# Kernel optimization log

Measured on AMD Instinct MI355X. Metric: run time of the kernel, lower is better.

Reference implementation:

```python
import jax, jax.numpy as jnp
from jax import lax
import numpy as np

B, T, ID, HD = 64, 256, 512, 1024

def setup_inputs() -> dict:
    key = jax.random.key(0)
    ks = jax.random.split(key, 5)
    s_i = 1.0 / np.sqrt(ID)
    s_h = 1.0 / np.sqrt(HD)
    return {
        'x': jax.random.normal(ks[0], (B, T, ID), jnp.float32),
        'Wi': jax.random.uniform(ks[1], (ID, 4 * HD), jnp.float32, -s_i, s_i),
        'bi': jax.random.uniform(ks[2], (4 * HD,), jnp.float32, -s_i, s_i),
        'Wh': jax.random.uniform(ks[3], (HD, 4 * HD), jnp.float32, -s_h, s_h),
        'bh': jax.random.uniform(ks[4], (4 * HD,), jnp.float32, -s_h, s_h),
    }

def reference(x, Wi, bi, Wh, bh):
    # x: [B, T, ID]; Wi: [ID, 4H]; Wh: [HD, 4H]
    b, t, _ = x.shape
    hd = Wh.shape[0]
    # Precompute input-to-hidden contribution for all timesteps: [T, B, 4H]
    gates_x = jnp.swapaxes(jnp.einsum('bti,ih->bth', x, Wi) + bi, 0, 1)

    def step(carry, gx):
        h, c = carry
        g = gx + h @ Wh + bh  # [B, 4H]
        f, i, a, o = jnp.split(g, 4, axis=-1)  # chunk order: F, I, A, O
        f = jax.nn.sigmoid(f)
        i = jax.nn.sigmoid(i)
        a = jnp.tanh(a)
        o = jax.nn.sigmoid(o)
        c = f * c + i * a
        h = o * jnp.tanh(c)
        return (h, c), h

    h0 = jnp.zeros((b, hd), x.dtype)
    c0 = jnp.zeros((b, hd), x.dtype)
    (hT, cT), hs = lax.scan(step, (h0, c0), gates_x)
    Q_all = jnp.swapaxes(hs, 0, 1)  # [B, T, HD]
    return (Q_all, hT, cT)
```

## Files before the change

kernel.cpp:

```cpp
#include <hip/hip_runtime.h>
#include <hip/hip_bf16.h>


#define B_  64
#define T_  256
#define ID_ 512
#define HD_ 1024
#define NG_ 4096
#define M1_ (B_ * T_)
#define NBLK 64
#define UPB  16

typedef __bf16 bf16x8 __attribute__((ext_vector_type(8)));
typedef float  f32x4  __attribute__((ext_vector_type(4)));
typedef int    i32x4  __attribute__((ext_vector_type(4)));
typedef short  s16x4  __attribute__((ext_vector_type(4)));

using bf16 = __hip_bfloat16;

__device__ __forceinline__ float sigmoid_fast(float x) {
    return 1.0f / (1.0f + __expf(-x));
}
__device__ __forceinline__ float tanh_fast(float x) {
    return 1.0f - 2.0f / (__expf(2.0f * x) + 1.0f);
}
__device__ __forceinline__ unsigned short bf16_bits(float x) {
    union { bf16 h; unsigned short u; } cv;
    cv.h = __float2bfloat16(x);
    return cv.u;
}
__device__ __forceinline__ bf16x8 as_bf16x8(i32x4 v) {
    union { i32x4 i; bf16x8 h; } cv;
    cv.i = v;
    return cv.h;
}

__device__ __forceinline__ void issue8(i32x4* dst, const bf16* gbase) {
    asm volatile(
        "global_load_dwordx4 %0, %8, off sc0 sc1\n\t"
        "global_load_dwordx4 %1, %8, off offset:64 sc0 sc1\n\t"
        "global_load_dwordx4 %2, %8, off offset:128 sc0 sc1\n\t"
        "global_load_dwordx4 %3, %8, off offset:192 sc0 sc1\n\t"
        "global_load_dwordx4 %4, %8, off offset:256 sc0 sc1\n\t"
        "global_load_dwordx4 %5, %8, off offset:320 sc0 sc1\n\t"
        "global_load_dwordx4 %6, %8, off offset:384 sc0 sc1\n\t"
        "global_load_dwordx4 %7, %8, off offset:448 sc0 sc1"
        : "=&v"(dst[0]), "=&v"(dst[1]), "=&v"(dst[2]), "=&v"(dst[3]),
          "=&v"(dst[4]), "=&v"(dst[5]), "=&v"(dst[6]), "=&v"(dst[7])
        : "v"(gbase));
}

__global__ __launch_bounds__(256) void prep_kernel(
    const float* __restrict__ x, const float* __restrict__ Wi,
    const float* __restrict__ Wh, bf16* __restrict__ xb,
    bf16* __restrict__ wiT, bf16* __restrict__ whT,
    bf16* __restrict__ hbuf, int* __restrict__ flags) {
    const int tid = blockIdx.x * 256 + threadIdx.x;

    if (tid < NBLK * 4 * 16) flags[tid] = 0;
    if (tid < (B_ * HD_) / 4)
        *reinterpret_cast<s16x4*>(hbuf + (size_t)tid * 4) = s16x4{0, 0, 0, 0};

    const float4 v = reinterpret_cast<const float4*>(x)[tid];
    bf16 tmp[4] = { __float2bfloat16(v.x), __float2bfloat16(v.y),
                    __float2bfloat16(v.z), __float2bfloat16(v.w) };
    *reinterpret_cast<s16x4*>(xb + 4 * (size_t)tid) =
        *reinterpret_cast<s16x4*>(tmp);

    {
        const int n = tid >> 9, k = tid & 511;
        wiT[tid] = __float2bfloat16(Wi[(size_t)k * NG_ + n]);
    }
    for (int e = 0; e < 2; ++e) {
        const int idx = 2 * tid + e;
        const int n = idx >> 10, k = idx & 1023;
        whT[idx] = __float2bfloat16(Wh[(size_t)k * NG_ + n]);
    }
}

__global__ __launch_bounds__(256) void gates_gemm_kernel(
    const bf16* __restrict__ xb, const bf16* __restrict__ wiT,
    const float* __restrict__ bi, const float* __restrict__ bh,
    bf16* __restrict__ gates3) {
    __shared__ __align__(16) bf16 As[128 * 40];
    __shared__ __align__(16) bf16 Bs[128 * 40];
    const int tid  = threadIdx.x;
    const int lane = tid & 63, wave = tid >> 6;
    const int wm = wave >> 1, wn = wave & 1;
    const int l15 = lane & 15, quad = lane >> 4;
    const int row0 = blockIdx.x * 128, col0 = blockIdx.y * 128;

    f32x4 acc[4][4];
    for (int i = 0; i < 4; ++i)
        for (int j = 0; j < 4; ++j) acc[i][j] = f32x4{0.f, 0.f, 0.f, 0.f};

    for (int kt = 0; kt < ID_ / 32; ++kt) {
        const int k0 = kt * 32;
        for (int L = tid; L < 512; L += 256) {
            const int r = L >> 2, s = L & 3;
            *reinterpret_cast<i32x4*>(&As[r * 40 + s * 8]) =
                *reinterpret_cast<const i32x4*>(xb + (size_t)(row0 + r) * ID_ + k0 + s * 8);
            *reinterpret_cast<i32x4*>(&Bs[r * 40 + s * 8]) =
                *reinterpret_cast<const i32x4*>(wiT + (size_t)(col0 + r) * ID_ + k0 + s * 8);
        }
        __syncthreads();
        bf16x8 af[4], bfv[4];
        for (int mt = 0; mt < 4; ++mt)
            af[mt] = *reinterpret_cast<const bf16x8*>(
                &As[(wm * 64 + mt * 16 + l15) * 40 + quad * 8]);
        for (int nt = 0; nt < 4; ++nt)
            bfv[nt] = *reinterpret_cast<const bf16x8*>(
                &Bs[(wn * 64 + nt * 16 + l15) * 40 + quad * 8]);
        for (int mt = 0; mt < 4; ++mt)
            for (int nt = 0; nt < 4; ++nt)
                acc[mt][nt] = __builtin_amdgcn_mfma_f32_16x16x32_bf16(
                    af[mt], bfv[nt], acc[mt][nt], 0, 0, 0);
        __syncthreads();
    }
    for (int mt = 0; mt < 4; ++mt) {
        for (int nt = 0; nt < 4; ++nt) {
            const int cg = col0 + wn * 64 + nt * 16 + l15;
            const int g = cg >> 10, u = cg & 1023;
            const int blk = u >> 4, ul = u & 15;
            const int q2 = ul >> 2, r2 = ul & 3;
            const int e = g * 4 + r2;
            const float bias = bi[cg] + bh[cg];
            for (int r = 0; r < 4; ++r) {
                const int rg = row0 + wm * 64 + mt * 16 + quad * 4 + r;
                const int b = rg >> 8, t = rg & 255;
                const int tid2 = (b >> 4) * 64 + q2 * 16 + (b & 15);
                gates3[(((size_t)t * NBLK + blk) * 256 + tid2) * 16 + e] =
                    __float2bfloat16(acc[mt][nt][r] + bias);
            }
        }
    }
}

__global__ __launch_bounds__(256, 1) void lstm_persistent_kernel(
    const bf16* __restrict__ gates3, const bf16* __restrict__ whT,
    bf16* __restrict__ hbuf, float* __restrict__ out, int* __restrict__ flags) {
    __shared__ __align__(16) bf16 whs[32 * 4 * 64 * 8];
    const int tid  = threadIdx.x;
    const int lane = tid & 63, w = tid >> 6;
    const int l15 = lane & 15, quad = lane >> 4;
    const int blk = blockIdx.x;

    for (int c = tid; c < 8192; c += 256) {
        const int kk = c >> 8, sel = (c >> 6) & 3, ln = c & 63;
        const size_t wrow = (size_t)(sel * HD_ + blk * UPB + (ln & 15));
        const int col = (ln >> 4) * 8 + kk * 32;
        *reinterpret_cast<i32x4*>(whs + (size_t)c * 8) =
            *reinterpret_cast<const i32x4*>(whT + wrow * HD_ + col);
    }
    __syncthreads();

    const bf16* wb = whs + (size_t)lane * 8;

    const int b = w * 16 + l15;
    float cs[4] = {0.f, 0.f, 0.f, 0.f};

    const volatile int* pf = (const volatile int*)(flags + lane);

    size_t gb0 = ((size_t)blk * 256 + tid) * 16;
    bf16x8 gxa_n = *reinterpret_cast<const bf16x8*>(gates3 + gb0);
    bf16x8 gxb_n = *reinterpret_cast<const bf16x8*>(gates3 + gb0 + 8);

    for (int t = 0; t < T_; ++t) {
        const bf16* hin  = hbuf + (size_t)(t & 1) * (B_ * HD_);
        bf16*       hout = hbuf + (size_t)((t + 1) & 1) * (B_ * HD_);
        const bf16x8 gxa = gxa_n, gxb = gxb_n;

        if (t > 0) {
            if (w == 0) {
                while (*pf < t) __builtin_amdgcn_s_sleep(2);
            }
            asm volatile("s_barrier" ::: "memory");
        }

        f32x4 aFe{0.f,0.f,0.f,0.f}, aFo{0.f,0.f,0.f,0.f};
        f32x4 aIe{0.f,0.f,0.f,0.f}, aIo{0.f,0.f,0.f,0.f};
        f32x4 aAe{0.f,0.f,0.f,0.f}, aAo{0.f,0.f,0.f,0.f};
        f32x4 aOe{0.f,0.f,0.f,0.f}, aOo{0.f,0.f,0.f,0.f};

        const bf16* hb_base = hin + (size_t)b * HD_ + quad * 8;
        i32x4 hbA[8], hbB[8];

        auto consume8 = [&](const i32x4* hbg, const int kkb) {
#pragma unroll
            for (int i = 0; i < 8; i += 2) {
                const int kk = kkb + i;
                const bf16* f0 = wb + (size_t)kk * 2048;
                const bf16* f1 = f0 + 2048;
                const bf16x8 he = as_bf16x8(hbg[i]);
                const bf16x8 ho = as_bf16x8(hbg[i + 1]);
                aFe = __builtin_amdgcn_mfma_f32_16x16x32_bf16(
                    *reinterpret_cast<const bf16x8*>(f0),        he, aFe, 0, 0, 0);
                aIe = __builtin_amdgcn_mfma_f32_16x16x32_bf16(
                    *reinterpret_cast<const bf16x8*>(f0 + 512),  he, aIe, 0, 0, 0);
                aAe = __builtin_amdgcn_mfma_f32_16x16x32_bf16(
                    *reinterpret_cast<const bf16x8*>(f0 + 1024), he, aAe, 0, 0, 0);
                aOe = __builtin_amdgcn_mfma_f32_16x16x32_bf16(
                    *reinterpret_cast<const bf16x8*>(f0 + 1536), he, aOe, 0, 0, 0);
                aFo = __builtin_amdgcn_mfma_f32_16x16x32_bf16(
                    *reinterpret_cast<const bf16x8*>(f1),        ho, aFo, 0, 0, 0);
                aIo = __builtin_amdgcn_mfma_f32_16x16x32_bf16(
                    *reinterpret_cast<const bf16x8*>(f1 + 512),  ho, aIo, 0, 0, 0);
                aAo = __builtin_amdgcn_mfma_f32_16x16x32_bf16(
                    *reinterpret_cast<const bf16x8*>(f1 + 1024), ho, aAo, 0, 0, 0);
                aOo = __builtin_amdgcn_mfma_f32_16x16x32_bf16(
                    *reinterpret_cast<const bf16x8*>(f1 + 1536), ho, aOo, 0, 0, 0);
            }
        };

        issue8(hbA, hb_base);
        issue8(hbB, hb_base + 8 * 32);
        asm volatile("s_waitcnt vmcnt(8)" ::: "memory");
        __builtin_amdgcn_sched_barrier(0);
        consume8(hbA, 0);
        issue8(hbA, hb_base + 16 * 32);
        asm volatile("s_waitcnt vmcnt(8)" ::: "memory");
        __builtin_amdgcn_sched_barrier(0);
        consume8(hbB, 8);
        issue8(hbB, hb_base + 24 * 32);
        asm volatile("s_waitcnt vmcnt(8)" ::: "memory");
        __builtin_amdgcn_sched_barrier(0);
        consume8(hbA, 16);
        asm volatile("s_waitcnt vmcnt(0)" ::: "memory");
        __builtin_amdgcn_sched_barrier(0);
        consume8(hbB, 24);

        const f32x4 accF = aFe + aFo;
        const f32x4 accI = aIe + aIo;
        const f32x4 accA = aAe + aAo;
        const f32x4 accO = aOe + aOo;
        float hs[4];
#pragma unroll
        for (int r = 0; r < 4; ++r) {
            const float fv = sigmoid_fast(accF[r] + (float)gxa[r]);
            const float iv = sigmoid_fast(accI[r] + (float)gxa[4 + r]);
            const float av = tanh_fast   (accA[r] + (float)gxb[r]);
            const float ov = sigmoid_fast(accO[r] + (float)gxb[4 + r]);
            cs[r] = fv * cs[r] + iv * av;
            hs[r] = ov * tanh_fast(cs[r]);
        }

        const int hidx = b * HD_ + blk * UPB + quad * 4;
        *reinterpret_cast<float4*>(
            out + ((size_t)b * T_ + t) * HD_ + blk * UPB + quad * 4) =
            make_float4(hs[0], hs[1], hs[2], hs[3]);
        if (t == T_ - 1) {
            *reinterpret_cast<float4*>(out + (size_t)M1_ * HD_ + hidx) =
                make_float4(hs[0], hs[1], hs[2], hs[3]);
            *reinterpret_cast<float4*>(
                out + (size_t)M1_ * HD_ + B_ * HD_ + hidx) =
                make_float4(cs[0], cs[1], cs[2], cs[3]);
        }
        if (t < T_ - 1) {
            const unsigned long long hp =
                (unsigned long long)bf16_bits(hs[0]) |
                ((unsigned long long)bf16_bits(hs[1]) << 16) |
                ((unsigned long long)bf16_bits(hs[2]) << 32) |
                ((unsigned long long)bf16_bits(hs[3]) << 48);
            *reinterpret_cast<volatile unsigned long long*>(hout + hidx) = hp;
            __asm__ __volatile__("s_waitcnt vmcnt(0)" ::: "memory");
            asm volatile("s_barrier" ::: "memory");
            if (tid == 0)
                *reinterpret_cast<volatile int*>(flags + blk) = t + 1;
            __asm__ __volatile__("" ::: "memory");
            const size_t gb = (((size_t)(t + 1) * NBLK + blk) * 256 + tid) * 16;
            gxa_n = *reinterpret_cast<const bf16x8*>(gates3 + gb);
            gxb_n = *reinterpret_cast<const bf16x8*>(gates3 + gb + 8);
        }
    }
}

extern "C" void kernel_launch(void* const* d_in, const int* in_sizes, int n_in,
                              void* d_out, int out_size, void* d_ws, size_t ws_size,
                              hipStream_t stream) {
    const float* x  = (const float*)d_in[0];
    const float* Wi = (const float*)d_in[1];
    const float* bi = (const float*)d_in[2];
    const float* Wh = (const float*)d_in[3];
    const float* bh = (const float*)d_in[4];
    float* out = (float*)d_out;

    char* ws = (char*)d_ws;
    size_t off = 0;
    bf16* xb     = (bf16*)(ws + off); off += (size_t)M1_ * ID_ * 2;
    bf16* wiT    = (bf16*)(ws + off); off += (size_t)NG_ * ID_ * 2;
    bf16* whT    = (bf16*)(ws + off); off += (size_t)NG_ * HD_ * 2;
    bf16* gates3 = (bf16*)(ws + off); off += (size_t)T_ * B_ * NG_ * 2;
    bf16* hbuf   = (bf16*)(ws + off); off += (size_t)2 * B_ * HD_ * 2;
    int* flags   = (int*)(ws + off);  off += (size_t)NBLK * 4 * 16 * 4;

    prep_kernel<<<8192, 256, 0, stream>>>(x, Wi, Wh, xb, wiT, whT, hbuf, flags);
    gates_gemm_kernel<<<dim3(128, 32), 256, 0, stream>>>(xb, wiT, bi, bh, gates3);

    lstm_persistent_kernel<<<dim3(NBLK), dim3(256), 0, stream>>>(
        gates3, whT, hbuf, out, flags);
}
```

Measured before the change: 2.050 ms.

## Halve persistent LSTM block to two waves, each handling two batch tiles

The recurrent kernel now runs 128 threads per block, and each wave processes two 16-row batch tiles. Each Wh fragment read from LDS is reused across both tiles, halving LDS weight traffic per MFMA. The precomputed-gate layout is rearranged to match, giving 32 elements per thread. The spin-wait also drops its s_sleep for lower wake-up latency on the flag. In exchange each wave does twice as much serial MFMA and activation work per step, needs more registers, and the block has fewer waves to hide latency.

```diff
diff --git a/kernel.cpp b/kernel.cpp
--- a/kernel.cpp
+++ b/kernel.cpp
@@ -123,20 +123,21 @@
             const int g = cg >> 10, u = cg & 1023;
             const int blk = u >> 4, ul = u & 15;
             const int q2 = ul >> 2, r2 = ul & 3;
-            const int e = g * 4 + r2;
             const float bias = bi[cg] + bh[cg];
             for (int r = 0; r < 4; ++r) {
                 const int rg = row0 + wm * 64 + mt * 16 + quad * 4 + r;
                 const int b = rg >> 8, t = rg & 255;
-                const int tid2 = (b >> 4) * 64 + q2 * 16 + (b & 15);
-                gates3[(((size_t)t * NBLK + blk) * 256 + tid2) * 16 + e] =
+                const int w2 = b >> 5, nt2 = (b >> 4) & 1;
+                const int tid2 = w2 * 64 + q2 * 16 + (b & 15);
+                const int e = nt2 * 16 + g * 4 + r2;
+                gates3[(((size_t)t * NBLK + blk) * 128 + tid2) * 32 + e] =
                     __float2bfloat16(acc[mt][nt][r] + bias);
             }
         }
     }
 }
 
-__global__ __launch_bounds__(256, 1) void lstm_persistent_kernel(
+__global__ __launch_bounds__(128, 1) void lstm_persistent_kernel(
     const bf16* __restrict__ gates3, const bf16* __restrict__ whT,
     bf16* __restrict__ hbuf, float* __restrict__ out, int* __restrict__ flags) {
     __shared__ __align__(16) bf16 whs[32 * 4 * 64 * 8];
@@ -145,7 +146,7 @@
     const int l15 = lane & 15, quad = lane >> 4;
     const int blk = blockIdx.x;
 
-    for (int c = tid; c < 8192; c += 256) {
+    for (int c = tid; c < 8192; c += 128) {
         const int kk = c >> 8, sel = (c >> 6) & 3, ln = c & 63;
         const size_t wrow = (size_t)(sel * HD_ + blk * UPB + (ln & 15));
         const int col = (ln >> 4) * 8 + kk * 32;
@@ -156,120 +157,140 @@
 
     const bf16* wb = whs + (size_t)lane * 8;
 
-    const int b = w * 16 + l15;
-    float cs[4] = {0.f, 0.f, 0.f, 0.f};
+    const int b0 = w * 32 + l15;
+    const int b1 = b0 + 16;
+    float cs0[4] = {0.f, 0.f, 0.f, 0.f};
+    float cs1[4] = {0.f, 0.f, 0.f, 0.f};
 
     const volatile int* pf = (const volatile int*)(flags + lane);
 
-    size_t gb0 = ((size_t)blk * 256 + tid) * 16;
-    bf16x8 gxa_n = *reinterpret_cast<const bf16x8*>(gates3 + gb0);
-    bf16x8 gxb_n = *reinterpret_cast<const bf16x8*>(gates3 + gb0 + 8);
+    const bf16* gx0 = gates3 + ((size_t)blk * 128 + tid) * 32;
+    bf16x8 g0n = *reinterpret_cast<const bf16x8*>(gx0);
+    bf16x8 g1n = *reinterpret_cast<const bf16x8*>(gx0 + 8);
+    bf16x8 g2n = *reinterpret_cast<const bf16x8*>(gx0 + 16);
+    bf16x8 g3n = *reinterpret_cast<const bf16x8*>(gx0 + 24);
 
     for (int t = 0; t < T_; ++t) {
         const bf16* hin  = hbuf + (size_t)(t & 1) * (B_ * HD_);
         bf16*       hout = hbuf + (size_t)((t + 1) & 1) * (B_ * HD_);
-        const bf16x8 gxa = gxa_n, gxb = gxb_n;
+        const bf16x8 g0 = g0n, g1 = g1n, g2 = g2n, g3 = g3n;
 
         if (t > 0) {
             if (w == 0) {
-                while (*pf < t) __builtin_amdgcn_s_sleep(2);
+                while (*pf < t) {}
             }
             asm volatile("s_barrier" ::: "memory");
         }
 
-        f32x4 aFe{0.f,0.f,0.f,0.f}, aFo{0.f,0.f,0.f,0.f};
-        f32x4 aIe{0.f,0.f,0.f,0.f}, aIo{0.f,0.f,0.f,0.f};
-        f32x4 aAe{0.f,0.f,0.f,0.f}, aAo{0.f,0.f,0.f,0.f};
-        f32x4 aOe{0.f,0.f,0.f,0.f}, aOo{0.f,0.f,0.f,0.f};
-
-        const bf16* hb_base = hin + (size_t)b * HD_ + quad * 8;
-        i32x4 hbA[8], hbB[8];
-
-        auto consume8 = [&](const i32x4* hbg, const int kkb) {
+        f32x4 aF0{0.f,0.f,0.f,0.f}, aI0{0.f,0.f,0.f,0.f};
+        f32x4 aA0{0.f,0.f,0.f,0.f}, aO0{0.f,0.f,0.f,0.f};
+        f32x4 aF1{0.f,0.f,0.f,0.f}, aI1{0.f,0.f,0.f,0.f};
+        f32x4 aA1{0.f,0.f,0.f,0.f}, aO1{0.f,0.f,0.f,0.f};
+
+        const bf16* base0 = hin + (size_t)b0 * HD_ + quad * 8;
+        const bf16* base1 = hin + (size_t)b1 * HD_ + quad * 8;
+        i32x4 hbA0[8], hbA1[8], hbB0[8], hbB1[8];
+
+        auto consumePair = [&](const i32x4* h0, const i32x4* h1, const int kkb) {
 #pragma unroll
-            for (int i = 0; i < 8; i += 2) {
+            for (int i = 0; i < 8; ++i) {
                 const int kk = kkb + i;
-                const bf16* f0 = wb + (size_t)kk * 2048;
-                const bf16* f1 = f0 + 2048;
-                const bf16x8 he = as_bf16x8(hbg[i]);
-                const bf16x8 ho = as_bf16x8(hbg[i + 1]);
-                aFe = __builtin_amdgcn_mfma_f32_16x16x32_bf16(
-                    *reinterpret_cast<const bf16x8*>(f0),        he, aFe, 0, 0, 0);
-                aIe = __builtin_amdgcn_mfma_f32_16x16x32_bf16(
-                    *reinterpret_cast<const bf16x8*>(f0 + 512),  he, aIe, 0, 0, 0);
-                aAe = __builtin_amdgcn_mfma_f32_16x16x32_bf16(
-                    *reinterpret_cast<const bf16x8*>(f0 + 1024), he, aAe, 0, 0, 0);
-                aOe = __builtin_amdgcn_mfma_f32_16x16x32_bf16(
-                    *reinterpret_cast<const bf16x8*>(f0 + 1536), he, aOe, 0, 0, 0);
-                aFo = __builtin_amdgcn_mfma_f32_16x16x32_bf16(
-                    *reinterpret_cast<const bf16x8*>(f1),        ho, aFo, 0, 0, 0);
-                aIo = __builtin_amdgcn_mfma_f32_16x16x32_bf16(
-                    *reinterpret_cast<const bf16x8*>(f1 + 512),  ho, aIo, 0, 0, 0);
-                aAo = __builtin_amdgcn_mfma_f32_16x16x32_bf16(
-                    *reinterpret_cast<const bf16x8*>(f1 + 1024), ho, aAo, 0, 0, 0);
-                aOo = __builtin_amdgcn_mfma_f32_16x16x32_bf16(
-                    *reinterpret_cast<const bf16x8*>(f1 + 1536), ho, aOo, 0, 0, 0);
+                const bf16* f = wb + (size_t)kk * 2048;
+                const bf16x8 wF = *reinterpret_cast<const bf16x8*>(f);
+                const bf16x8 wI = *reinterpret_cast<const bf16x8*>(f + 512);
+                const bf16x8 wA = *reinterpret_cast<const bf16x8*>(f + 1024);
+                const bf16x8 wO = *reinterpret_cast<const bf16x8*>(f + 1536);
+                const bf16x8 h0v = as_bf16x8(h0[i]);
+                const bf16x8 h1v = as_bf16x8(h1[i]);
+                aF0 = __builtin_amdgcn_mfma_f32_16x16x32_bf16(wF, h0v, aF0, 0, 0, 0);
+                aF1 = __builtin_amdgcn_mfma_f32_16x16x32_bf16(wF, h1v, aF1, 0, 0, 0);
+                aI0 = __builtin_amdgcn_mfma_f32_16x16x32_bf16(wI, h0v, aI0, 0, 0, 0);
+                aI1 = __builtin_amdgcn_mfma_f32_16x16x32_bf16(wI, h1v, aI1, 0, 0, 0);
+                aA0 = __builtin_amdgcn_mfma_f32_16x16x32_bf16(wA, h0v, aA0, 0, 0, 0);
+                aA1 = __builtin_amdgcn_mfma_f32_16x16x32_bf16(wA, h1v, aA1, 0, 0, 0);
+                aO0 = __builtin_amdgcn_mfma_f32_16x16x32_bf16(wO, h0v, aO0, 0, 0, 0);
+                aO1 = __builtin_amdgcn_mfma_f32_16x16x32_bf16(wO, h1v, aO1, 0, 0, 0);
             }
         };
 
-        issue8(hbA, hb_base);
-        issue8(hbB, hb_base + 8 * 32);
-        asm volatile("s_waitcnt vmcnt(8)" ::: "memory");
+        issue8(hbA0, base0);        issue8(hbA1, base1);
+        issue8(hbB0, base0 + 256);  issue8(hbB1, base1 + 256);
+        asm volatile("s_waitcnt vmcnt(16)" ::: "memory");
         __builtin_amdgcn_sched_barrier(0);
-        consume8(hbA, 0);
-        issue8(hbA, hb_base + 16 * 32);
-        asm volatile("s_waitcnt vmcnt(8)" ::: "memory");
+        consumePair(hbA0, hbA1, 0);
+        issue8(hbA0, base0 + 512);  issue8(hbA1, base1 + 512);
+        asm volatile("s_waitcnt vmcnt(16)" ::: "memory");
         __builtin_amdgcn_sched_barrier(0);
-        consume8(hbB, 8);
-        issue8(hbB, hb_base + 24 * 32);
-        asm volatile("s_waitcnt vmcnt(8)" ::: "memory");
+        consumePair(hbB0, hbB1, 8);
+        issue8(hbB0, base0 + 768);  issue8(hbB1, base1 + 768);
+        asm volatile("s_waitcnt vmcnt(16)" ::: "memory");
         __builtin_amdgcn_sched_barrier(0);
-        consume8(hbA, 16);
+        consumePair(hbA0, hbA1, 16);
         asm volatile("s_waitcnt vmcnt(0)" ::: "memory");
         __builtin_amdgcn_sched_barrier(0);
-        consume8(hbB, 24);
-
-        const f32x4 accF = aFe + aFo;
-        const f32x4 accI = aIe + aIo;
-        const f32x4 accA = aAe + aAo;
-        const f32x4 accO = aOe + aOo;
-        float hs[4];
+        consumePair(hbB0, hbB1, 24);
+
+        float hs0[4], hs1[4];
 #pragma unroll
         for (int r = 0; r < 4; ++r) {
-            const float fv = sigmoid_fast(accF[r] + (float)gxa[r]);
-            const float iv = sigmoid_fast(accI[r] + (float)gxa[4 + r]);
-            const float av = tanh_fast   (accA[r] + (float)gxb[r]);
-            const float ov = sigmoid_fast(accO[r] + (float)gxb[4 + r]);
-            cs[r] = fv * cs[r] + iv * av;
-            hs[r] = ov * tanh_fast(cs[r]);
-        }
-
-        const int hidx = b * HD_ + blk * UPB + quad * 4;
+            const float F0 = sigmoid_fast(aF0[r] + (float)g0[r]);
+            const float I0 = sigmoid_fast(aI0[r] + (float)g0[4 + r]);
+            const float A0 = tanh_fast   (aA0[r] + (float)g1[r]);
+            const float O0 = sigmoid_fast(aO0[r] + (float)g1[4 + r]);
+            cs0[r] = F0 * cs0[r] + I0 * A0;
+            hs0[r] = O0 * tanh_fast(cs0[r]);
+            const float F1 = sigmoid_fast(aF1[r] + (float)g2[r]);
+            const float I1 = sigmoid_fast(aI1[r] + (float)g2[4 + r]);
+            const float A1 = tanh_fast   (aA1[r] + (float)g3[r]);
+            const float O1 = sigmoid_fast(aO1[r] + (float)g3[4 + r]);
+            cs1[r] = F1 * cs1[r] + I1 * A1;
+            hs1[r] = O1 * tanh_fast(cs1[r]);
+        }
+
+        const int hidx0 = b0 * HD_ + blk * UPB + quad * 4;
+        const int hidx1 = b1 * HD_ + blk * UPB + quad * 4;
         *reinterpret_cast<float4*>(
-            out + ((size_t)b * T_ + t) * HD_ + blk * UPB + quad * 4) =
-            make_float4(hs[0], hs[1], hs[2], hs[3]);
+            out + ((size_t)b0 * T_ + t) * HD_ + blk * UPB + quad * 4) =
+            make_float4(hs0[0], hs0[1], hs0[2], hs0[3]);
+        *reinterpret_cast<float4*>(
+            out + ((size_t)b1 * T_ + t) * HD_ + blk * UPB + quad * 4) =
+            make_float4(hs1[0], hs1[1], hs1[2], hs1[3]);
         if (t == T_ - 1) {
-            *reinterpret_cast<float4*>(out + (size_t)M1_ * HD_ + hidx) =
-                make_float4(hs[0], hs[1], hs[2], hs[3]);
+            *reinterpret_cast<float4*>(out + (size_t)M1_ * HD_ + hidx0) =
+                make_float4(hs0[0], hs0[1], hs0[2], hs0[3]);
+            *reinterpret_cast<float4*>(out + (size_t)M1_ * HD_ + hidx1) =
+                make_float4(hs1[0], hs1[1], hs1[2], hs1[3]);
             *reinterpret_cast<float4*>(
-                out + (size_t)M1_ * HD_ + B_ * HD_ + hidx) =
-                make_float4(cs[0], cs[1], cs[2], cs[3]);
+                out + (size_t)M1_ * HD_ + B_ * HD_ + hidx0) =
+                make_float4(cs0[0], cs0[1], cs0[2], cs0[3]);
+            *reinterpret_cast<float4*>(
+                out + (size_t)M1_ * HD_ + B_ * HD_ + hidx1) =
+                make_float4(cs1[0], cs1[1], cs1[2], cs1[3]);
         }
         if (t < T_ - 1) {
-            const unsigned long long hp =
-                (unsigned long long)bf16_bits(hs[0]) |
-                ((unsigned long long)bf16_bits(hs[1]) << 16) |
-                ((unsigned long long)bf16_bits(hs[2]) << 32) |
-                ((unsigned long long)bf16_bits(hs[3]) << 48);
-            *reinterpret_cast<volatile unsigned long long*>(hout + hidx) = hp;
+            const unsigned long long hp0 =
+                (unsigned long long)bf16_bits(hs0[0]) |
+                ((unsigned long long)bf16_bits(hs0[1]) << 16) |
+                ((unsigned long long)bf16_bits(hs0[2]) << 32) |
+                ((unsigned long long)bf16_bits(hs0[3]) << 48);
+            const unsigned long long hp1 =
+                (unsigned long long)bf16_bits(hs1[0]) |
+                ((unsigned long long)bf16_bits(hs1[1]) << 16) |
+                ((unsigned long long)bf16_bits(hs1[2]) << 32) |
+                ((unsigned long long)bf16_bits(hs1[3]) << 48);
+            *reinterpret_cast<volatile unsigned long long*>(hout + hidx0) = hp0;
+            *reinterpret_cast<volatile unsigned long long*>(hout + hidx1) = hp1;
             __asm__ __volatile__("s_waitcnt vmcnt(0)" ::: "memory");
             asm volatile("s_barrier" ::: "memory");
             if (tid == 0)
                 *reinterpret_cast<volatile int*>(flags + blk) = t + 1;
             __asm__ __volatile__("" ::: "memory");
-            const size_t gb = (((size_t)(t + 1) * NBLK + blk) * 256 + tid) * 16;
-            gxa_n = *reinterpret_cast<const bf16x8*>(gates3 + gb);
-            gxb_n = *reinterpret_cast<const bf16x8*>(gates3 + gb + 8);
+            const bf16* gxp = gates3 +
+                (((size_t)(t + 1) * NBLK + blk) * 128 + tid) * 32;
+            g0n = *reinterpret_cast<const bf16x8*>(gxp);
+            g1n = *reinterpret_cast<const bf16x8*>(gxp + 8);
+            g2n = *reinterpret_cast<const bf16x8*>(gxp + 16);
+            g3n = *reinterpret_cast<const bf16x8*>(gxp + 24);
         }
     }
 }
@@ -296,6 +317,6 @@
     prep_kernel<<<8192, 256, 0, stream>>>(x, Wi, Wh, xb, wiT, whT, hbuf, flags);
     gates_gemm_kernel<<<dim3(128, 32), 256, 0, stream>>>(xb, wiT, bi, bh, gates3);
 
-    lstm_persistent_kernel<<<dim3(NBLK), dim3(256), 0, stream>>>(
+    lstm_persistent_kernel<<<dim3(NBLK), dim3(128), 0, stream>>>(
         gates3, whT, hbuf, out, flags);
 }
```

New measurement: 2.372 ms. 15.7% more time.
